# Kernel optimization log

Measured on AMD Instinct MI355X. Metric: run time of the kernel, lower is better.

## Reference

```python
import jax, jax.numpy as jnp
import numpy as np

ALPHA = 0.0  # module init alpha
BETA = 1.0   # default beta in set_target_with_data


def setup_inputs() -> dict:
    key = jax.random.key(0)
    k1, k2, k3, k4 = jax.random.split(key, 4)
    B, H, KP, N, D = 4, 16, 512, 4096, 64
    return {
        "K": jax.random.normal(k1, (B, H, KP, D), dtype=jnp.float32),
        "V": jax.random.normal(k2, (B, H, KP, D), dtype=jnp.float32),
        "xk": jax.random.normal(k3, (B, H, N, D), dtype=jnp.float32),
        "xv": jax.random.normal(k4, (B, H, N, D), dtype=jnp.float32),
    }


def reference(K, V, xk, xv):
    # set_target_with_data with dist_metric='dot', beta=1.0, beta2=None
    # dists: (B, H, k, n) = K @ xk^T
    dists = jnp.einsum('bhkd,bhnd->bhkn', K, xk)
    # softmax over the memory-slot axis (dim=-2)
    dk = jax.nn.softmax(BETA * dists, axis=-2)
    # normalize over the data axis (dim=-1)
    dkx = dk / jnp.sum(dk, axis=-1, keepdims=True)
    # weighted readout of data queries/values
    K_target = jnp.einsum('bhkn,bhnd->bhkd', dkx, xk)
    V_target = jnp.einsum('bhkn,bhnd->bhkd', dkx, xv)
    # set_target: grads used by maximize-SGD update
    gK = (1.0 - ALPHA) * (K_target - K)
    gV = (1.0 - ALPHA) * (V_target - V)
    return jnp.stack((gK, gV), axis=0)  # (2, B, H, k, d)
```

## Files before the change

### kernel.cpp

```cpp
#include <hip/hip_runtime.h>
#include <hip/hip_bf16.h>

typedef __bf16 bf16_t;
typedef __attribute__((ext_vector_type(8))) __bf16 bf16x8;
typedef __attribute__((ext_vector_type(4))) float f32x4;

#define BH 64
#define KP 512
#define NN 4096
#define DD 64
#define GSZ (BH * KP * DD)

#define MFMA16(a, b, c) __builtin_amdgcn_mfma_f32_16x16x32_bf16((a), (b), (c), 0, 0, 0)

__device__ __forceinline__ bf16x8 cvt8v(const f32x4 lo, const f32x4 hi) {
  bf16x8 r;
  r[0] = (bf16_t)lo[0]; r[1] = (bf16_t)lo[1]; r[2] = (bf16_t)lo[2]; r[3] = (bf16_t)lo[3];
  r[4] = (bf16_t)hi[0]; r[5] = (bf16_t)hi[1]; r[6] = (bf16_t)hi[2]; r[7] = (bf16_t)hi[3];
  return r;
}
__device__ __forceinline__ bf16x8 cvt8(const float* __restrict__ p) {
  return cvt8v(*(const f32x4*)p, *(const f32x4*)(p + 4));
}

__device__ __forceinline__ void stage16(bf16_t* lds_base, const bf16_t* gsrc) {
  __builtin_amdgcn_global_load_lds(
      (const __attribute__((address_space(1))) void*)gsrc,
      (__attribute__((address_space(3))) void*)lds_base, 16, 0, 0);
}

__global__ __launch_bounds__(256) void hop_prep(
    const float* __restrict__ xk, const float* __restrict__ xv,
    bf16_t* __restrict__ xk16, bf16_t* __restrict__ xkT16, bf16_t* __restrict__ xvT16)
{
  __shared__ __align__(16) bf16_t T[64 * 72];
  const int t = threadIdx.x;
  const int n0 = blockIdx.x * 64;
  const int bh = blockIdx.y;
  const int row = t >> 2;
  const int d0  = (t & 3) * 16;
  const int dcol = t >> 2;
  const int nb   = (t & 3) * 16;
  const size_t gb  = (size_t)bh * NN * DD;
  const size_t gbT = (size_t)bh * DD * NN;

  {
    const float* src = xk + gb + (size_t)(n0 + row) * DD + d0;
    const f32x4 a0 = *(const f32x4*)(src);
    const f32x4 a1 = *(const f32x4*)(src + 4);
    const f32x4 a2 = *(const f32x4*)(src + 8);
    const f32x4 a3 = *(const f32x4*)(src + 12);
    const bf16x8 lo = cvt8v(a0, a1), hi = cvt8v(a2, a3);
    bf16_t* dn = xk16 + gb + (size_t)(n0 + row) * DD + d0;
    *(bf16x8*)(dn)     = lo;
    *(bf16x8*)(dn + 8) = hi;
    *(bf16x8*)(T + row * 72 + d0)     = lo;
    *(bf16x8*)(T + row * 72 + d0 + 8) = hi;
  }
  __syncthreads();
  {
    bf16x8 o0, o1;
    #pragma unroll
    for (int j = 0; j < 8; j++) o0[j] = T[(nb + j) * 72 + dcol];
    #pragma unroll
    for (int j = 0; j < 8; j++) o1[j] = T[(nb + 8 + j) * 72 + dcol];
    bf16_t* dT = xkT16 + gbT + (size_t)dcol * NN + n0 + nb;
    *(bf16x8*)(dT)     = o0;
    *(bf16x8*)(dT + 8) = o1;
  }
  __syncthreads();
  {
    const float* src = xv + gb + (size_t)(n0 + row) * DD + d0;
    const f32x4 a0 = *(const f32x4*)(src);
    const f32x4 a1 = *(const f32x4*)(src + 4);
    const f32x4 a2 = *(const f32x4*)(src + 8);
    const f32x4 a3 = *(const f32x4*)(src + 12);
    *(bf16x8*)(T + row * 72 + d0)     = cvt8v(a0, a1);
    *(bf16x8*)(T + row * 72 + d0 + 8) = cvt8v(a2, a3);
  }
  __syncthreads();
  {
    bf16x8 o0, o1;
    #pragma unroll
    for (int j = 0; j < 8; j++) o0[j] = T[(nb + j) * 72 + dcol];
    #pragma unroll
    for (int j = 0; j < 8; j++) o1[j] = T[(nb + 8 + j) * 72 + dcol];
    bf16_t* dT = xvT16 + gbT + (size_t)dcol * NN + n0 + nb;
    *(bf16x8*)(dT)     = o0;
    *(bf16x8*)(dT + 8) = o1;
  }
}

__global__ __launch_bounds__(256) void hop_pass1(
    const float* __restrict__ Km, const bf16_t* __restrict__ xk16,
    float* __restrict__ inv_colsum)
{
  __shared__ __align__(16) bf16_t Ks[128 * 72];

  const int tid  = threadIdx.x;
  const int wave = tid >> 6, lane = tid & 63;
  const int col  = lane & 15, quad = lane >> 4;
  const int bid  = blockIdx.x;
  const int bh   = (bid & 7) + 8 * ((bid >> 3) & 7);
  const int n0   = (bid >> 6) * 256 + wave * 64;

  const float*  Kb   = Km   + (size_t)bh * KP * DD;
  const bf16_t* xkb  = xk16 + (size_t)bh * NN * DD;

  bf16x8 bf[4][2];
  #pragma unroll
  for (int nsub = 0; nsub < 4; nsub++) {
    const bf16_t* p = xkb + (size_t)(n0 + nsub * 16 + col) * DD + quad * 8;
    bf[nsub][0] = *(const bf16x8*)(p);
    bf[nsub][1] = *(const bf16x8*)(p + 32);
  }

  float colacc[4] = {0.f, 0.f, 0.f, 0.f};
  const int srow = tid >> 1, sdo = (tid & 1) * 32;

  for (int kc = 0; kc < KP; kc += 128) {
    __syncthreads();
    const float* src = Kb + (size_t)(kc + srow) * DD + sdo;
    #pragma unroll
    for (int u = 0; u < 4; u++) {
      const f32x4 p0 = *(const f32x4*)(src + 8 * u);
      const f32x4 p1 = *(const f32x4*)(src + 8 * u + 4);
      *(bf16x8*)(Ks + srow * 72 + sdo + 8 * u) = cvt8v(p0, p1);
    }
    __syncthreads();
    #pragma unroll
    for (int ks = 0; ks < 8; ks++) {
      const bf16x8 a0 = *(const bf16x8*)(Ks + (ks * 16 + col) * 72 + quad * 8);
      const bf16x8 a1 = *(const bf16x8*)(Ks + (ks * 16 + col) * 72 + 32 + quad * 8);
      #pragma unroll
      for (int nsub = 0; nsub < 4; nsub++) {
        f32x4 c = {0.f, 0.f, 0.f, 0.f};
        c = MFMA16(a0, bf[nsub][0], c);
        c = MFMA16(a1, bf[nsub][1], c);
        colacc[nsub] += __expf(c[0]) + __expf(c[1]) + __expf(c[2]) + __expf(c[3]);
      }
    }
  }
  #pragma unroll
  for (int nsub = 0; nsub < 4; nsub++) {
    colacc[nsub] += __shfl_xor(colacc[nsub], 16, 64);
    colacc[nsub] += __shfl_xor(colacc[nsub], 32, 64);
  }
  float v = colacc[0];
  v = (quad == 1) ? colacc[1] : v;
  v = (quad == 2) ? colacc[2] : v;
  v = (quad == 3) ? colacc[3] : v;
  inv_colsum[bh * NN + n0 + quad * 16 + col] = 1.0f / v;
}

#define NT 64
#define PW 72

__global__ __launch_bounds__(256) void hop_pass2(
    const float* __restrict__ Km, const float* __restrict__ Vm,
    const bf16_t* __restrict__ xk16, const bf16_t* __restrict__ xkT16,
    const bf16_t* __restrict__ xvT16,
    const float* __restrict__ inv_colsum, float* __restrict__ out)
{
  __shared__ __align__(16) bf16_t xks[2][NT * DD];
  __shared__ __align__(16) bf16_t xkT[2][DD * NT];
  __shared__ __align__(16) bf16_t xvT[2][DD * NT];
  __shared__ __align__(16) bf16_t wt[4][16 * PW];

  const int tid  = threadIdx.x;
  const int wave = tid >> 6, lane = tid & 63;
  const int col  = lane & 15, quad = lane >> 4;
  const int bid  = blockIdx.x;
  const int bh   = (bid & 7) + 8 * ((bid >> 3) & 7);
  const int k0   = (bid >> 6) * 64 + wave * 16;

  const float*  Kb   = Km    + (size_t)bh * KP * DD;
  const float*  Vb   = Vm    + (size_t)bh * KP * DD;
  const bf16_t* xkb  = xk16  + (size_t)bh * NN * DD;
  const bf16_t* xkTb = xkT16 + (size_t)bh * DD * NN;
  const bf16_t* xvTb = xvT16 + (size_t)bh * DD * NN;
  const float*  inv  = inv_colsum + bh * NN;

  const bf16x8 ak0 = cvt8(Kb + (size_t)(k0 + col) * DD + quad * 8);
  const bf16x8 ak1 = cvt8(Kb + (size_t)(k0 + col) * DD + 32 + quad * 8);

  f32x4 accK[4], accV[4];
  #pragma unroll
  for (int i = 0; i < 4; i++) {
    accK[i] = (f32x4){0.f, 0.f, 0.f, 0.f};
    accV[i] = (f32x4){0.f, 0.f, 0.f, 0.f};
  }
  float rows_part = 0.f;

  const int srl = lane >> 3;
  const int r0  = wave * 16 + srl;
  const int r1  = r0 + 8;
  const int sb  = ((lane & 7) ^ srl) * 8;
  const int lb0 = (wave * 2 + 0) * 512;
  const int lb1 = (wave * 2 + 1) * 512;

  stage16(&xks[0][lb0], xkb + (size_t)r0 * DD + sb);
  stage16(&xks[0][lb1], xkb + (size_t)r1 * DD + sb);
  stage16(&xkT[0][lb0], xkTb + (size_t)r0 * NN + sb);
  stage16(&xkT[0][lb1], xkTb + (size_t)r1 * NN + sb);
  stage16(&xvT[0][lb0], xvTb + (size_t)r0 * NN + sb);
  stage16(&xvT[0][lb1], xvTb + (size_t)r1 * NN + sb);
  __syncthreads();

  int cur = 0;
  for (int n0 = 0; n0 < NN; n0 += NT) {
    if (n0 + NT < NN) {
      const int nx = n0 + NT;
      const int nb = cur ^ 1;
      stage16(&xks[nb][lb0], xkb + (size_t)(nx + r0) * DD + sb);
      stage16(&xks[nb][lb1], xkb + (size_t)(nx + r1) * DD + sb);
      stage16(&xkT[nb][lb0], xkTb + (size_t)r0 * NN + nx + sb);
      stage16(&xkT[nb][lb1], xkTb + (size_t)r1 * NN + nx + sb);
      stage16(&xvT[nb][lb0], xvTb + (size_t)r0 * NN + nx + sb);
      stage16(&xvT[nb][lb1], xvTb + (size_t)r1 * NN + nx + sb);
    }

    float ic[4];
    #pragma unroll
    for (int ns = 0; ns < 4; ns++) ic[ns] = inv[n0 + ns * 16 + col];

    const int key = col & 7;

    f32x4 s[4];
    #pragma unroll
    for (int ns = 0; ns < 4; ns++) {
      const bf16_t* bp = &xks[cur][(ns * 16 + col) * DD];
      const bf16x8 b0 = *(const bf16x8*)(bp + 8 * (quad ^ key));
      const bf16x8 b1 = *(const bf16x8*)(bp + 8 * ((quad + 4) ^ key));
      f32x4 c = {0.f, 0.f, 0.f, 0.f};
      c = MFMA16(ak0, b0, c);
      c = MFMA16(ak1, b1, c);
      s[ns] = c;
    }
    bf16_t* wr = wt[wave];
    #pragma unroll
    for (int ns = 0; ns < 4; ns++) {
      #pragma unroll
      for (int r = 0; r < 4; r++)
        wr[(quad * 4 + r) * PW + ns * 16 + col] = (bf16_t)(__expf(s[ns][r]) * ic[ns]);
    }
    const bf16x8 wa0 = *(const bf16x8*)(wr + col * PW + quad * 8);
    const bf16x8 wa1 = *(const bf16x8*)(wr + col * PW + 32 + quad * 8);
    #pragma unroll
    for (int j = 0; j < 8; j++) rows_part += (float)wa0[j] + (float)wa1[j];

    #pragma unroll
    for (int dt = 0; dt < 4; dt++) {
      const int d = dt * 16 + col;
      const bf16_t* kp = &xkT[cur][d * NT];
      const bf16_t* vp = &xvT[cur][d * NT];
      const bf16x8 bk0 = *(const bf16x8*)(kp + 8 * (quad ^ key));
      const bf16x8 bk1 = *(const bf16x8*)(kp + 8 * ((quad + 4) ^ key));
      const bf16x8 bv0 = *(const bf16x8*)(vp + 8 * (quad ^ key));
      const bf16x8 bv1 = *(const bf16x8*)(vp + 8 * ((quad + 4) ^ key));
      accK[dt] = MFMA16(wa0, bk0, accK[dt]);
      accK[dt] = MFMA16(wa1, bk1, accK[dt]);
      accV[dt] = MFMA16(wa0, bv0, accV[dt]);
      accV[dt] = MFMA16(wa1, bv1, accV[dt]);
    }

    __syncthreads();
    cur ^= 1;
  }

  float rs = rows_part;
  rs += __shfl_xor(rs, 16, 64);
  rs += __shfl_xor(rs, 32, 64);
  float invrs[4];
  #pragma unroll
  for (int r = 0; r < 4; r++) invrs[r] = 1.0f / __shfl(rs, quad * 4 + r, 64);

  const size_t base = (size_t)bh * KP * DD;
  #pragma unroll
  for (int dt = 0; dt < 4; dt++) {
    #pragma unroll
    for (int r = 0; r < 4; r++) {
      const int k = k0 + quad * 4 + r;
      const int d = dt * 16 + col;
      const size_t idx = base + (size_t)k * DD + d;
      out[idx]       = accK[dt][r] * invrs[r] - Kb[(size_t)k * DD + d];
      out[GSZ + idx] = accV[dt][r] * invrs[r] - Vb[(size_t)k * DD + d];
    }
  }
}

__global__ __launch_bounds__(256) void hop_pass1_fb(
    const float* __restrict__ Km, const float* __restrict__ xk,
    float* __restrict__ inv_colsum)
{
  __shared__ __align__(16) bf16_t Ks[128 * 72];
  const int tid  = threadIdx.x;
  const int wave = tid >> 6, lane = tid & 63;
  const int col  = lane & 15, quad = lane >> 4;
  const int bh = blockIdx.y;
  const int n0 = blockIdx.x * 256 + wave * 64;
  const float* Kb  = Km + (size_t)bh * KP * DD;
  const float* xkb = xk + (size_t)bh * NN * DD;
  bf16x8 bf[4][2];
  #pragma unroll
  for (int nsub = 0; nsub < 4; nsub++) {
    const float* p = xkb + (size_t)(n0 + nsub * 16 + col) * DD + quad * 8;
    bf[nsub][0] = cvt8(p);
    bf[nsub][1] = cvt8(p + 32);
  }
  float colacc[4] = {0.f, 0.f, 0.f, 0.f};
  const int srow = tid >> 1, sdo = (tid & 1) * 32;
  for (int kc = 0; kc < KP; kc += 128) {
    __syncthreads();
    const float* src = Kb + (size_t)(kc + srow) * DD + sdo;
    #pragma unroll
    for (int u = 0; u < 4; u++) {
      const f32x4 p0 = *(const f32x4*)(src + 8 * u);
      const f32x4 p1 = *(const f32x4*)(src + 8 * u + 4);
      *(bf16x8*)(Ks + srow * 72 + sdo + 8 * u) = cvt8v(p0, p1);
    }
    __syncthreads();
    #pragma unroll
    for (int ks = 0; ks < 8; ks++) {
      const bf16x8 a0 = *(const bf16x8*)(Ks + (ks * 16 + col) * 72 + quad * 8);
      const bf16x8 a1 = *(const bf16x8*)(Ks + (ks * 16 + col) * 72 + 32 + quad * 8);
      #pragma unroll
      for (int nsub = 0; nsub < 4; nsub++) {
        f32x4 c = {0.f, 0.f, 0.f, 0.f};
        c = MFMA16(a0, bf[nsub][0], c);
        c = MFMA16(a1, bf[nsub][1], c);
        colacc[nsub] += __expf(c[0]) + __expf(c[1]) + __expf(c[2]) + __expf(c[3]);
      }
    }
  }
  #pragma unroll
  for (int nsub = 0; nsub < 4; nsub++) {
    colacc[nsub] += __shfl_xor(colacc[nsub], 16, 64);
    colacc[nsub] += __shfl_xor(colacc[nsub], 32, 64);
  }
  float v = colacc[0];
  v = (quad == 1) ? colacc[1] : v;
  v = (quad == 2) ? colacc[2] : v;
  v = (quad == 3) ? colacc[3] : v;
  inv_colsum[bh * NN + n0 + quad * 16 + col] = 1.0f / v;
}

__global__ __launch_bounds__(256) void hop_pass2_fb(
    const float* __restrict__ Km, const float* __restrict__ Vm,
    const float* __restrict__ xk, const float* __restrict__ xv,
    const float* __restrict__ inv_colsum, float* __restrict__ out)
{
  __shared__ __align__(16) bf16_t xksf[NT * PW];
  __shared__ __align__(16) bf16_t xkTf[DD * NT];
  __shared__ __align__(16) bf16_t xvTf[DD * NT];
  __shared__ __align__(16) bf16_t wtf[4][16 * PW];

  const int tid  = threadIdx.x;
  const int wave = tid >> 6, lane = tid & 63;
  const int col  = lane & 15, quad = lane >> 4;
  const int bh   = blockIdx.x >> 3;
  const int k0   = (blockIdx.x & 7) * 64 + wave * 16;

  const float* Kb  = Km + (size_t)bh * KP * DD;
  const float* Vb  = Vm + (size_t)bh * KP * DD;
  const float* xkb = xk + (size_t)bh * NN * DD;
  const float* xvb = xv + (size_t)bh * NN * DD;
  const float* inv = inv_colsum + bh * NN;

  const bf16x8 ak0 = cvt8(Kb + (size_t)(k0 + col) * DD + quad * 8);
  const bf16x8 ak1 = cvt8(Kb + (size_t)(k0 + col) * DD + 32 + quad * 8);

  f32x4 accK[4], accV[4];
  #pragma unroll
  for (int i = 0; i < 4; i++) {
    accK[i] = (f32x4){0.f, 0.f, 0.f, 0.f};
    accV[i] = (f32x4){0.f, 0.f, 0.f, 0.f};
  }
  float rows_part = 0.f;

  const int sn = tid >> 2;
  const int sd = (tid & 3) * 16;
  const int shi = sn >> 3, slo = sn & 7;

  for (int n0 = 0; n0 < NN; n0 += NT) {
    f32x4 gk[4], gv[4];
    #pragma unroll
    for (int u = 0; u < 4; u++) {
      gk[u] = *(const f32x4*)(xkb + (size_t)(n0 + sn) * DD + sd + 4 * u);
      gv[u] = *(const f32x4*)(xvb + (size_t)(n0 + sn) * DD + sd + 4 * u);
    }
    float ic[4];
    #pragma unroll
    for (int nsub = 0; nsub < 4; nsub++) ic[nsub] = inv[n0 + nsub * 16 + col];

    __syncthreads();
    *(bf16x8*)(xksf + sn * PW + sd)     = cvt8v(gk[0], gk[1]);
    *(bf16x8*)(xksf + sn * PW + sd + 8) = cvt8v(gk[2], gk[3]);
    #pragma unroll
    for (int j = 0; j < 16; j++) {
      const int d   = sd + j;
      const int off = d * NT + (((shi) ^ (d >> 3)) << 3) + slo;
      xkTf[off] = (bf16_t)gk[j >> 2][j & 3];
      xvTf[off] = (bf16_t)gv[j >> 2][j & 3];
    }
    __syncthreads();

    f32x4 s[4];
    #pragma unroll
    for (int nsub = 0; nsub < 4; nsub++) {
      const bf16x8 b0 = *(const bf16x8*)(xksf + (nsub * 16 + col) * PW + quad * 8);
      const bf16x8 b1 = *(const bf16x8*)(xksf + (nsub * 16 + col) * PW + 32 + quad * 8);
      f32x4 c = {0.f, 0.f, 0.f, 0.f};
      c = MFMA16(ak0, b0, c);
      c = MFMA16(ak1, b1, c);
      s[nsub] = c;
    }
    bf16_t* wr = wtf[wave];
    #pragma unroll
    for (int nsub = 0; nsub < 4; nsub++) {
      #pragma unroll
      for (int r = 0; r < 4; r++)
        wr[(quad * 4 + r) * PW + nsub * 16 + col] = (bf16_t)(__expf(s[nsub][r]) * ic[nsub]);
    }
    const bf16x8 wa0 = *(const bf16x8*)(wr + col * PW + quad * 8);
    const bf16x8 wa1 = *(const bf16x8*)(wr + col * PW + 32 + quad * 8);
    #pragma unroll
    for (int j = 0; j < 8; j++) rows_part += (float)wa0[j] + (float)wa1[j];

    #pragma unroll
    for (int dt = 0; dt < 4; dt++) {
      const int d = dt * 16 + col, dhi = d >> 3;
      const bf16x8 bk0 = *(const bf16x8*)(xkTf + d * NT + ((quad ^ dhi) << 3));
      const bf16x8 bk1 = *(const bf16x8*)(xkTf + d * NT + (((4 + quad) ^ dhi) << 3));
      const bf16x8 bv0 = *(const bf16x8*)(xvTf + d * NT + ((quad ^ dhi) << 3));
      const bf16x8 bv1 = *(const bf16x8*)(xvTf + d * NT + (((4 + quad) ^ dhi) << 3));
      accK[dt] = MFMA16(wa0, bk0, accK[dt]);
      accK[dt] = MFMA16(wa1, bk1, accK[dt]);
      accV[dt] = MFMA16(wa0, bv0, accV[dt]);
      accV[dt] = MFMA16(wa1, bv1, accV[dt]);
    }
  }

  float rs = rows_part;
  rs += __shfl_xor(rs, 16, 64);
  rs += __shfl_xor(rs, 32, 64);
  float invrs[4];
  #pragma unroll
  for (int r = 0; r < 4; r++) invrs[r] = 1.0f / __shfl(rs, quad * 4 + r, 64);

  const size_t base = (size_t)bh * KP * DD;
  #pragma unroll
  for (int dt = 0; dt < 4; dt++) {
    #pragma unroll
    for (int r = 0; r < 4; r++) {
      const int k = k0 + quad * 4 + r;
      const int d = dt * 16 + col;
      const size_t idx = base + (size_t)k * DD + d;
      out[idx]       = accK[dt][r] * invrs[r] - Kb[(size_t)k * DD + d];
      out[GSZ + idx] = accV[dt][r] * invrs[r] - Vb[(size_t)k * DD + d];
    }
  }
}

extern "C" void kernel_launch(void* const* d_in, const int* in_sizes, int n_in,
                              void* d_out, int out_size, void* d_ws, size_t ws_size,
                              hipStream_t stream)
{
  (void)in_sizes; (void)n_in; (void)out_size;
  const float* Km = (const float*)d_in[0];
  const float* Vm = (const float*)d_in[1];
  const float* xk = (const float*)d_in[2];
  const float* xv = (const float*)d_in[3];
  float* out = (float*)d_out;
  float* inv_colsum = (float*)d_ws;

  const size_t SCRE = (size_t)BH * NN * DD;
  const size_t NEED = (size_t)BH * NN * sizeof(float) + 3 * SCRE * sizeof(bf16_t);

  if (ws_size >= NEED) {
    bf16_t* xk16  = (bf16_t*)((char*)d_ws + (size_t)BH * NN * sizeof(float));
    bf16_t* xkT16 = xk16 + SCRE;
    bf16_t* xvT16 = xkT16 + SCRE;
    hop_prep<<<dim3(NN / 64, BH), 256, 0, stream>>>(xk, xv, xk16, xkT16, xvT16);
    hop_pass1<<<dim3((NN / 256) * BH), 256, 0, stream>>>(Km, xk16, inv_colsum);
    hop_pass2<<<dim3(BH * (KP / 64)), 256, 0, stream>>>(Km, Vm, xk16, xkT16, xvT16,
                                                        inv_colsum, out);
  } else {
    hop_pass1_fb<<<dim3(NN / 256, BH), 256, 0, stream>>>(Km, xk, inv_colsum);
    hop_pass2_fb<<<dim3(BH * (KP / 64)), 256, 0, stream>>>(Km, Vm, xk, xv,
                                                           inv_colsum, out);
  }
}
```

Before: 306.4 us.

## Fuse bf16 prep/transpose into pass1 with whole-K LDS staging

Merges the xk/xv bf16 conversion and transpose kernel into the column-sum pass. Each block handles 512 data rows of one head, converts and transposes them, then stages all of K in LDS once and computes the exp column sums. This drops one kernel launch and stops K from being reloaded per 256-column block. In exchange it uses a much larger LDS footprint (about 72KB), which lowers occupancy. The prep work also runs serially before the MFMA work inside each block, and the grid shrinks to 512 blocks.

```diff
diff --git a/kernel.cpp b/kernel.cpp
--- a/kernel.cpp
+++ b/kernel.cpp
@@ -29,128 +29,133 @@
       (__attribute__((address_space(3))) void*)lds_base, 16, 0, 0);
 }
 
-__global__ __launch_bounds__(256) void hop_prep(
-    const float* __restrict__ xk, const float* __restrict__ xv,
-    bf16_t* __restrict__ xk16, bf16_t* __restrict__ xkT16, bf16_t* __restrict__ xvT16)
+__global__ __launch_bounds__(256) void hop_pass1f(
+    const float* __restrict__ Km, const float* __restrict__ xk,
+    const float* __restrict__ xv,
+    bf16_t* __restrict__ xk16, bf16_t* __restrict__ xkT16,
+    bf16_t* __restrict__ xvT16, float* __restrict__ inv_colsum)
 {
-  __shared__ __align__(16) bf16_t T[64 * 72];
-  const int t = threadIdx.x;
-  const int n0 = blockIdx.x * 64;
-  const int bh = blockIdx.y;
-  const int row = t >> 2;
-  const int d0  = (t & 3) * 16;
-  const int dcol = t >> 2;
-  const int nb   = (t & 3) * 16;
-  const size_t gb  = (size_t)bh * NN * DD;
-  const size_t gbT = (size_t)bh * DD * NN;
-
-  {
-    const float* src = xk + gb + (size_t)(n0 + row) * DD + d0;
-    const f32x4 a0 = *(const f32x4*)(src);
-    const f32x4 a1 = *(const f32x4*)(src + 4);
-    const f32x4 a2 = *(const f32x4*)(src + 8);
-    const f32x4 a3 = *(const f32x4*)(src + 12);
-    const bf16x8 lo = cvt8v(a0, a1), hi = cvt8v(a2, a3);
-    bf16_t* dn = xk16 + gb + (size_t)(n0 + row) * DD + d0;
-    *(bf16x8*)(dn)     = lo;
-    *(bf16x8*)(dn + 8) = hi;
-    *(bf16x8*)(T + row * 72 + d0)     = lo;
-    *(bf16x8*)(T + row * 72 + d0 + 8) = hi;
-  }
-  __syncthreads();
-  {
-    bf16x8 o0, o1;
-    #pragma unroll
-    for (int j = 0; j < 8; j++) o0[j] = T[(nb + j) * 72 + dcol];
-    #pragma unroll
-    for (int j = 0; j < 8; j++) o1[j] = T[(nb + 8 + j) * 72 + dcol];
-    bf16_t* dT = xkT16 + gbT + (size_t)dcol * NN + n0 + nb;
-    *(bf16x8*)(dT)     = o0;
-    *(bf16x8*)(dT + 8) = o1;
-  }
-  __syncthreads();
-  {
-    const float* src = xv + gb + (size_t)(n0 + row) * DD + d0;
-    const f32x4 a0 = *(const f32x4*)(src);
-    const f32x4 a1 = *(const f32x4*)(src + 4);
-    const f32x4 a2 = *(const f32x4*)(src + 8);
-    const f32x4 a3 = *(const f32x4*)(src + 12);
-    *(bf16x8*)(T + row * 72 + d0)     = cvt8v(a0, a1);
-    *(bf16x8*)(T + row * 72 + d0 + 8) = cvt8v(a2, a3);
-  }
-  __syncthreads();
-  {
-    bf16x8 o0, o1;
-    #pragma unroll
-    for (int j = 0; j < 8; j++) o0[j] = T[(nb + j) * 72 + dcol];
-    #pragma unroll
-    for (int j = 0; j < 8; j++) o1[j] = T[(nb + 8 + j) * 72 + dcol];
-    bf16_t* dT = xvT16 + gbT + (size_t)dcol * NN + n0 + nb;
-    *(bf16x8*)(dT)     = o0;
-    *(bf16x8*)(dT + 8) = o1;
-  }
-}
-
-__global__ __launch_bounds__(256) void hop_pass1(
-    const float* __restrict__ Km, const bf16_t* __restrict__ xk16,
-    float* __restrict__ inv_colsum)
-{
-  __shared__ __align__(16) bf16_t Ks[128 * 72];
+  __shared__ __align__(16) bf16_t Ks[512 * 72];
 
   const int tid  = threadIdx.x;
   const int wave = tid >> 6, lane = tid & 63;
   const int col  = lane & 15, quad = lane >> 4;
   const int bid  = blockIdx.x;
   const int bh   = (bid & 7) + 8 * ((bid >> 3) & 7);
-  const int n0   = (bid >> 6) * 256 + wave * 64;
-
-  const float*  Kb   = Km   + (size_t)bh * KP * DD;
-  const bf16_t* xkb  = xk16 + (size_t)bh * NN * DD;
-
-  bf16x8 bf[4][2];
-  #pragma unroll
-  for (int nsub = 0; nsub < 4; nsub++) {
-    const bf16_t* p = xkb + (size_t)(n0 + nsub * 16 + col) * DD + quad * 8;
-    bf[nsub][0] = *(const bf16x8*)(p);
-    bf[nsub][1] = *(const bf16x8*)(p + 32);
-  }
-
-  float colacc[4] = {0.f, 0.f, 0.f, 0.f};
-  const int srow = tid >> 1, sdo = (tid & 1) * 32;
-
-  for (int kc = 0; kc < KP; kc += 128) {
-    __syncthreads();
-    const float* src = Kb + (size_t)(kc + srow) * DD + sdo;
-    #pragma unroll
-    for (int u = 0; u < 4; u++) {
-      const f32x4 p0 = *(const f32x4*)(src + 8 * u);
-      const f32x4 p1 = *(const f32x4*)(src + 8 * u + 4);
-      *(bf16x8*)(Ks + srow * 72 + sdo + 8 * u) = cvt8v(p0, p1);
-    }
-    __syncthreads();
-    #pragma unroll
-    for (int ks = 0; ks < 8; ks++) {
+  const int nblk = (bid >> 6) * 512;
+
+  const float* Kb  = Km + (size_t)bh * KP * DD;
+  const float* xkb = xk + (size_t)bh * NN * DD + (size_t)nblk * DD;
+  const float* xvb = xv + (size_t)bh * NN * DD + (size_t)nblk * DD;
+  bf16_t* xk16b = xk16  + (size_t)bh * NN * DD + (size_t)nblk * DD;
+  bf16_t* xkTb  = xkT16 + (size_t)bh * DD * NN + nblk;
+  bf16_t* xvTb  = xvT16 + (size_t)bh * DD * NN + nblk;
+
+  bf16_t* T = Ks;
+
+  const int row  = tid >> 2;
+  const int d0   = (tid & 3) * 16;
+  const int dcol = tid >> 2;
+  const int nb   = (tid & 3) * 16;
+
+  for (int b = 0; b < 8; b++) {
+    {
+      const float* src = xkb + (size_t)(b * 64 + row) * DD + d0;
+      const f32x4 a0 = *(const f32x4*)(src);
+      const f32x4 a1 = *(const f32x4*)(src + 4);
+      const f32x4 a2 = *(const f32x4*)(src + 8);
+      const f32x4 a3 = *(const f32x4*)(src + 12);
+      const bf16x8 lo = cvt8v(a0, a1), hi = cvt8v(a2, a3);
+      bf16_t* dn = xk16b + (size_t)(b * 64 + row) * DD + d0;
+      *(bf16x8*)(dn)     = lo;
+      *(bf16x8*)(dn + 8) = hi;
+      *(bf16x8*)(T + row * 72 + d0)     = lo;
+      *(bf16x8*)(T + row * 72 + d0 + 8) = hi;
+    }
+    __syncthreads();
+    {
+      bf16x8 o0, o1;
+      #pragma unroll
+      for (int j = 0; j < 8; j++) o0[j] = T[(nb + j) * 72 + dcol];
+      #pragma unroll
+      for (int j = 0; j < 8; j++) o1[j] = T[(nb + 8 + j) * 72 + dcol];
+      bf16_t* dT = xkTb + (size_t)dcol * NN + b * 64 + nb;
+      *(bf16x8*)(dT)     = o0;
+      *(bf16x8*)(dT + 8) = o1;
+    }
+    __syncthreads();
+    {
+      const float* src = xvb + (size_t)(b * 64 + row) * DD + d0;
+      const f32x4 a0 = *(const f32x4*)(src);
+      const f32x4 a1 = *(const f32x4*)(src + 4);
+      const f32x4 a2 = *(const f32x4*)(src + 8);
+      const f32x4 a3 = *(const f32x4*)(src + 12);
+      *(bf16x8*)(T + row * 72 + d0)     = cvt8v(a0, a1);
+      *(bf16x8*)(T + row * 72 + d0 + 8) = cvt8v(a2, a3);
+    }
+    __syncthreads();
+    {
+      bf16x8 o0, o1;
+      #pragma unroll
+      for (int j = 0; j < 8; j++) o0[j] = T[(nb + j) * 72 + dcol];
+      #pragma unroll
+      for (int j = 0; j < 8; j++) o1[j] = T[(nb + 8 + j) * 72 + dcol];
+      bf16_t* dT = xvTb + (size_t)dcol * NN + b * 64 + nb;
+      *(bf16x8*)(dT)     = o0;
+      *(bf16x8*)(dT + 8) = o1;
+    }
+    __syncthreads();
+  }
+
+  {
+    const int srow = tid >> 1, sdo = (tid & 1) * 32;
+    #pragma unroll
+    for (int kc = 0; kc < KP; kc += 128) {
+      const float* src = Kb + (size_t)(kc + srow) * DD + sdo;
+      #pragma unroll
+      for (int u = 0; u < 4; u++) {
+        const f32x4 p0 = *(const f32x4*)(src + 8 * u);
+        const f32x4 p1 = *(const f32x4*)(src + 8 * u + 4);
+        *(bf16x8*)(Ks + (size_t)(kc + srow) * 72 + sdo + 8 * u) = cvt8v(p0, p1);
+      }
+    }
+  }
+  __syncthreads();
+
+  #pragma unroll
+  for (int t = 0; t < 2; t++) {
+    const int n0 = wave * 128 + t * 64;
+    bf16x8 bfr[4][2];
+    #pragma unroll
+    for (int nsub = 0; nsub < 4; nsub++) {
+      const bf16_t* p = xk16b + (size_t)(n0 + nsub * 16 + col) * DD + quad * 8;
+      bfr[nsub][0] = *(const bf16x8*)(p);
+      bfr[nsub][1] = *(const bf16x8*)(p + 32);
+    }
+    float colacc[4] = {0.f, 0.f, 0.f, 0.f};
+    #pragma unroll 4
+    for (int ks = 0; ks < 32; ks++) {
       const bf16x8 a0 = *(const bf16x8*)(Ks + (ks * 16 + col) * 72 + quad * 8);
       const bf16x8 a1 = *(const bf16x8*)(Ks + (ks * 16 + col) * 72 + 32 + quad * 8);
       #pragma unroll
       for (int nsub = 0; nsub < 4; nsub++) {
         f32x4 c = {0.f, 0.f, 0.f, 0.f};
-        c = MFMA16(a0, bf[nsub][0], c);
-        c = MFMA16(a1, bf[nsub][1], c);
+        c = MFMA16(a0, bfr[nsub][0], c);
+        c = MFMA16(a1, bfr[nsub][1], c);
         colacc[nsub] += __expf(c[0]) + __expf(c[1]) + __expf(c[2]) + __expf(c[3]);
       }
     }
-  }
-  #pragma unroll
-  for (int nsub = 0; nsub < 4; nsub++) {
-    colacc[nsub] += __shfl_xor(colacc[nsub], 16, 64);
-    colacc[nsub] += __shfl_xor(colacc[nsub], 32, 64);
-  }
-  float v = colacc[0];
-  v = (quad == 1) ? colacc[1] : v;
-  v = (quad == 2) ? colacc[2] : v;
-  v = (quad == 3) ? colacc[3] : v;
-  inv_colsum[bh * NN + n0 + quad * 16 + col] = 1.0f / v;
+    #pragma unroll
+    for (int nsub = 0; nsub < 4; nsub++) {
+      colacc[nsub] += __shfl_xor(colacc[nsub], 16, 64);
+      colacc[nsub] += __shfl_xor(colacc[nsub], 32, 64);
+    }
+    float v = colacc[0];
+    v = (quad == 1) ? colacc[1] : v;
+    v = (quad == 2) ? colacc[2] : v;
+    v = (quad == 3) ? colacc[3] : v;
+    inv_colsum[bh * NN + nblk + n0 + quad * 16 + col] = 1.0f / v;
+  }
 }
 
 #define NT 64
@@ -211,13 +216,13 @@
   for (int n0 = 0; n0 < NN; n0 += NT) {
     if (n0 + NT < NN) {
       const int nx = n0 + NT;
-      const int nb = cur ^ 1;
-      stage16(&xks[nb][lb0], xkb + (size_t)(nx + r0) * DD + sb);
-      stage16(&xks[nb][lb1], xkb + (size_t)(nx + r1) * DD + sb);
-      stage16(&xkT[nb][lb0], xkTb + (size_t)r0 * NN + nx + sb);
-      stage16(&xkT[nb][lb1], xkTb + (size_t)r1 * NN + nx + sb);
-      stage16(&xvT[nb][lb0], xvTb + (size_t)r0 * NN + nx + sb);
-      stage16(&xvT[nb][lb1], xvTb + (size_t)r1 * NN + nx + sb);
+      const int nb2 = cur ^ 1;
+      stage16(&xks[nb2][lb0], xkb + (size_t)(nx + r0) * DD + sb);
+      stage16(&xks[nb2][lb1], xkb + (size_t)(nx + r1) * DD + sb);
+      stage16(&xkT[nb2][lb0], xkTb + (size_t)r0 * NN + nx + sb);
+      stage16(&xkT[nb2][lb1], xkTb + (size_t)r1 * NN + nx + sb);
+      stage16(&xvT[nb2][lb0], xvTb + (size_t)r0 * NN + nx + sb);
+      stage16(&xvT[nb2][lb1], xvTb + (size_t)r1 * NN + nx + sb);
     }
 
     float ic[4];
@@ -481,8 +486,8 @@
     bf16_t* xk16  = (bf16_t*)((char*)d_ws + (size_t)BH * NN * sizeof(float));
     bf16_t* xkT16 = xk16 + SCRE;
     bf16_t* xvT16 = xkT16 + SCRE;
-    hop_prep<<<dim3(NN / 64, BH), 256, 0, stream>>>(xk, xv, xk16, xkT16, xvT16);
-    hop_pass1<<<dim3((NN / 256) * BH), 256, 0, stream>>>(Km, xk16, inv_colsum);
+    hop_pass1f<<<dim3(512), 256, 0, stream>>>(Km, xk, xv, xk16, xkT16, xvT16,
+                                              inv_colsum);
     hop_pass2<<<dim3(BH * (KP / 64)), 256, 0, stream>>>(Km, Vm, xk16, xkT16, xvT16,
                                                         inv_colsum, out);
   } else {
```

Result: no change. 311.3 us (+1.6%).

## Use 32x32 MFMA in pass2 with register permlane weight transpose

Applied to the files above, without the earlier changes.

Rewrites the second pass to use 32x32x16 bf16 MFMA with each wave covering 32 memory rows. Scores are computed transposed so the exp weights can be rearranged into the A-operand layout with v_permlane32_swap instead of round-tripping through LDS. Each block handles 128 rows, which halves how often data tiles are reloaded per row, but also halves the grid size and raises register use.

```diff
diff --git a/kernel.cpp b/kernel.cpp
--- a/kernel.cpp
+++ b/kernel.cpp
@@ -4,6 +4,7 @@
 typedef __bf16 bf16_t;
 typedef __attribute__((ext_vector_type(8))) __bf16 bf16x8;
 typedef __attribute__((ext_vector_type(4))) float f32x4;
+typedef __attribute__((ext_vector_type(16))) float f32x16;
 
 #define BH 64
 #define KP 512
@@ -12,6 +13,7 @@
 #define GSZ (BH * KP * DD)
 
 #define MFMA16(a, b, c) __builtin_amdgcn_mfma_f32_16x16x32_bf16((a), (b), (c), 0, 0, 0)
+#define MFMA32(a, b, c) __builtin_amdgcn_mfma_f32_32x32x16_bf16((a), (b), (c), 0, 0, 0)
 
 __device__ __forceinline__ bf16x8 cvt8v(const f32x4 lo, const f32x4 hi) {
   bf16x8 r;
@@ -21,6 +23,11 @@
 }
 __device__ __forceinline__ bf16x8 cvt8(const float* __restrict__ p) {
   return cvt8v(*(const f32x4*)p, *(const f32x4*)(p + 4));
+}
+__device__ __forceinline__ unsigned pack2(float a, float b) {
+  union { bf16_t h[2]; unsigned u; } x;
+  x.h[0] = (bf16_t)a; x.h[1] = (bf16_t)b;
+  return x.u;
 }
 
 __device__ __forceinline__ void stage16(bf16_t* lds_base, const bf16_t* gsrc) {
@@ -154,7 +161,6 @@
 }
 
 #define NT 64
-#define PW 72
 
 __global__ __launch_bounds__(256) void hop_pass2(
     const float* __restrict__ Km, const float* __restrict__ Vm,
@@ -165,14 +171,16 @@
   __shared__ __align__(16) bf16_t xks[2][NT * DD];
   __shared__ __align__(16) bf16_t xkT[2][DD * NT];
   __shared__ __align__(16) bf16_t xvT[2][DD * NT];
-  __shared__ __align__(16) bf16_t wt[4][16 * PW];
+  __shared__ float rows_lds[4][32];
 
   const int tid  = threadIdx.x;
   const int wave = tid >> 6, lane = tid & 63;
-  const int col  = lane & 15, quad = lane >> 4;
+  const int col  = lane & 31, hi = lane >> 5;
   const int bid  = blockIdx.x;
-  const int bh   = (bid & 7) + 8 * ((bid >> 3) & 7);
-  const int k0   = (bid >> 6) * 64 + wave * 16;
+  const int m    = bid >> 3;
+  const int bh   = (bid & 7) + 8 * (m >> 2);
+  const int kblk = m & 3;
+  const int k0w  = kblk * 128 + wave * 32;
 
   const float*  Kb   = Km    + (size_t)bh * KP * DD;
   const float*  Vb   = Vm    + (size_t)bh * KP * DD;
@@ -181,16 +189,18 @@
   const bf16_t* xvTb = xvT16 + (size_t)bh * DD * NN;
   const float*  inv  = inv_colsum + bh * NN;
 
-  const bf16x8 ak0 = cvt8(Kb + (size_t)(k0 + col) * DD + quad * 8);
-  const bf16x8 ak1 = cvt8(Kb + (size_t)(k0 + col) * DD + 32 + quad * 8);
-
-  f32x4 accK[4], accV[4];
-  #pragma unroll
-  for (int i = 0; i < 4; i++) {
-    accK[i] = (f32x4){0.f, 0.f, 0.f, 0.f};
-    accV[i] = (f32x4){0.f, 0.f, 0.f, 0.f};
-  }
-  float rows_part = 0.f;
+  bf16x8 bk[4];
+  #pragma unroll
+  for (int t = 0; t < 4; t++)
+    bk[t] = cvt8(Kb + (size_t)(k0w + col) * DD + t * 16 + hi * 8);
+
+  f32x16 accK[2], accV[2];
+  #pragma unroll
+  for (int i = 0; i < 2; i++) {
+    #pragma unroll
+    for (int r = 0; r < 16; r++) { accK[i][r] = 0.f; accV[i][r] = 0.f; }
+  }
+  float rowacc = 0.f;
 
   const int srl = lane >> 3;
   const int r0  = wave * 16 + srl;
@@ -211,83 +221,92 @@
   for (int n0 = 0; n0 < NN; n0 += NT) {
     if (n0 + NT < NN) {
       const int nx = n0 + NT;
-      const int nb = cur ^ 1;
-      stage16(&xks[nb][lb0], xkb + (size_t)(nx + r0) * DD + sb);
-      stage16(&xks[nb][lb1], xkb + (size_t)(nx + r1) * DD + sb);
-      stage16(&xkT[nb][lb0], xkTb + (size_t)r0 * NN + nx + sb);
-      stage16(&xkT[nb][lb1], xkTb + (size_t)r1 * NN + nx + sb);
-      stage16(&xvT[nb][lb0], xvTb + (size_t)r0 * NN + nx + sb);
-      stage16(&xvT[nb][lb1], xvTb + (size_t)r1 * NN + nx + sb);
-    }
-
-    float ic[4];
-    #pragma unroll
-    for (int ns = 0; ns < 4; ns++) ic[ns] = inv[n0 + ns * 16 + col];
-
-    const int key = col & 7;
-
-    f32x4 s[4];
-    #pragma unroll
-    for (int ns = 0; ns < 4; ns++) {
-      const bf16_t* bp = &xks[cur][(ns * 16 + col) * DD];
-      const bf16x8 b0 = *(const bf16x8*)(bp + 8 * (quad ^ key));
-      const bf16x8 b1 = *(const bf16x8*)(bp + 8 * ((quad + 4) ^ key));
-      f32x4 c = {0.f, 0.f, 0.f, 0.f};
-      c = MFMA16(ak0, b0, c);
-      c = MFMA16(ak1, b1, c);
-      s[ns] = c;
-    }
-    bf16_t* wr = wt[wave];
-    #pragma unroll
-    for (int ns = 0; ns < 4; ns++) {
-      #pragma unroll
-      for (int r = 0; r < 4; r++)
-        wr[(quad * 4 + r) * PW + ns * 16 + col] = (bf16_t)(__expf(s[ns][r]) * ic[ns]);
-    }
-    const bf16x8 wa0 = *(const bf16x8*)(wr + col * PW + quad * 8);
-    const bf16x8 wa1 = *(const bf16x8*)(wr + col * PW + 32 + quad * 8);
-    #pragma unroll
-    for (int j = 0; j < 8; j++) rows_part += (float)wa0[j] + (float)wa1[j];
-
-    #pragma unroll
-    for (int dt = 0; dt < 4; dt++) {
-      const int d = dt * 16 + col;
-      const bf16_t* kp = &xkT[cur][d * NT];
-      const bf16_t* vp = &xvT[cur][d * NT];
-      const bf16x8 bk0 = *(const bf16x8*)(kp + 8 * (quad ^ key));
-      const bf16x8 bk1 = *(const bf16x8*)(kp + 8 * ((quad + 4) ^ key));
-      const bf16x8 bv0 = *(const bf16x8*)(vp + 8 * (quad ^ key));
-      const bf16x8 bv1 = *(const bf16x8*)(vp + 8 * ((quad + 4) ^ key));
-      accK[dt] = MFMA16(wa0, bk0, accK[dt]);
-      accK[dt] = MFMA16(wa1, bk1, accK[dt]);
-      accV[dt] = MFMA16(wa0, bv0, accV[dt]);
-      accV[dt] = MFMA16(wa1, bv1, accV[dt]);
+      const int nb2 = cur ^ 1;
+      stage16(&xks[nb2][lb0], xkb + (size_t)(nx + r0) * DD + sb);
+      stage16(&xks[nb2][lb1], xkb + (size_t)(nx + r1) * DD + sb);
+      stage16(&xkT[nb2][lb0], xkTb + (size_t)r0 * NN + nx + sb);
+      stage16(&xkT[nb2][lb1], xkTb + (size_t)r1 * NN + nx + sb);
+      stage16(&xvT[nb2][lb0], xvTb + (size_t)r0 * NN + nx + sb);
+      stage16(&xvT[nb2][lb1], xvTb + (size_t)r1 * NN + nx + sb);
+    }
+
+    const bf16_t* xs = xks[cur];
+    bf16x8 wa[4];
+
+    #pragma unroll
+    for (int nh = 0; nh < 2; nh++) {
+      f32x4 icv[4];
+      #pragma unroll
+      for (int q = 0; q < 4; q++)
+        icv[q] = *(const f32x4*)(inv + n0 + 32 * nh + 8 * q + 4 * hi);
+
+      const int n  = nh * 32 + col;
+      const int rb = n * DD;
+      f32x16 s;
+      #pragma unroll
+      for (int r = 0; r < 16; r++) s[r] = 0.f;
+      #pragma unroll
+      for (int t = 0; t < 4; t++) {
+        const bf16x8 a = *(const bf16x8*)(xs + rb + (((2 * t + hi) ^ (n & 7)) << 3));
+        s = MFMA32(a, bk[t], s);
+      }
+      #pragma unroll
+      for (int b = 0; b < 2; b++) {
+        float p[8];
+        #pragma unroll
+        for (int j = 0; j < 8; j++)
+          p[j] = __expf(s[8 * b + j]) * icv[2 * b + (j >> 2)][j & 3];
+        rowacc += ((p[0] + p[1]) + (p[2] + p[3])) + ((p[4] + p[5]) + (p[6] + p[7]));
+        unsigned q0a = pack2(p[0], p[1]), q0b = pack2(p[2], p[3]);
+        unsigned q1a = pack2(p[4], p[5]), q1b = pack2(p[6], p[7]);
+        asm("v_permlane32_swap_b32 %0, %1" : "+v"(q0a), "+v"(q1a));
+        asm("v_permlane32_swap_b32 %0, %1" : "+v"(q0b), "+v"(q1b));
+        union { unsigned u[4]; bf16x8 v; } f;
+        f.u[0] = q0a; f.u[1] = q0b; f.u[2] = q1a; f.u[3] = q1b;
+        wa[nh * 2 + b] = f.v;
+      }
+    }
+
+    #pragma unroll
+    for (int dg = 0; dg < 2; dg++) {
+      const int d   = dg * 32 + col;
+      const int rbd = d * NT;
+      const bf16_t* kp = xkT[cur];
+      const bf16_t* vp = xvT[cur];
+      #pragma unroll
+      for (int c = 0; c < 4; c++) {
+        const int off = rbd + (((2 * c + hi) ^ (d & 7)) << 3);
+        const bf16x8 bkf = *(const bf16x8*)(kp + off);
+        const bf16x8 bvf = *(const bf16x8*)(vp + off);
+        accK[dg] = MFMA32(wa[c], bkf, accK[dg]);
+        accV[dg] = MFMA32(wa[c], bvf, accV[dg]);
+      }
     }
 
     __syncthreads();
     cur ^= 1;
   }
 
-  float rs = rows_part;
-  rs += __shfl_xor(rs, 16, 64);
-  rs += __shfl_xor(rs, 32, 64);
-  float invrs[4];
-  #pragma unroll
-  for (int r = 0; r < 4; r++) invrs[r] = 1.0f / __shfl(rs, quad * 4 + r, 64);
+  rowacc += __shfl_xor(rowacc, 32, 64);
+  rows_lds[wave][col] = 1.0f / rowacc;
 
   const size_t base = (size_t)bh * KP * DD;
   #pragma unroll
-  for (int dt = 0; dt < 4; dt++) {
-    #pragma unroll
-    for (int r = 0; r < 4; r++) {
-      const int k = k0 + quad * 4 + r;
-      const int d = dt * 16 + col;
+  for (int dg = 0; dg < 2; dg++) {
+    #pragma unroll
+    for (int r = 0; r < 16; r++) {
+      const int kw = (r & 3) + 8 * (r >> 2) + 4 * hi;
+      const float invr = rows_lds[wave][kw];
+      const int k = k0w + kw;
+      const int d = dg * 32 + col;
       const size_t idx = base + (size_t)k * DD + d;
-      out[idx]       = accK[dt][r] * invrs[r] - Kb[(size_t)k * DD + d];
-      out[GSZ + idx] = accV[dt][r] * invrs[r] - Vb[(size_t)k * DD + d];
-    }
-  }
-}
+      out[idx]       = accK[dg][r] * invr - Kb[(size_t)k * DD + d];
+      out[GSZ + idx] = accV[dg][r] * invr - Vb[(size_t)k * DD + d];
+    }
+  }
+}
+
+#define PW 72
 
 __global__ __launch_bounds__(256) void hop_pass1_fb(
     const float* __restrict__ Km, const float* __restrict__ xk,
@@ -483,8 +502,8 @@
     bf16_t* xvT16 = xkT16 + SCRE;
     hop_prep<<<dim3(NN / 64, BH), 256, 0, stream>>>(xk, xv, xk16, xkT16, xvT16);
     hop_pass1<<<dim3((NN / 256) * BH), 256, 0, stream>>>(Km, xk16, inv_colsum);
-    hop_pass2<<<dim3(BH * (KP / 64)), 256, 0, stream>>>(Km, Vm, xk16, xkT16, xvT16,
-                                                        inv_colsum, out);
+    hop_pass2<<<dim3(BH * 4), 256, 0, stream>>>(Km, Vm, xk16, xkT16, xvT16,
+                                                inv_colsum, out);
   } else {
     hop_pass1_fb<<<dim3(NN / 256, BH), 256, 0, stream>>>(Km, xk, inv_colsum);
     hop_pass2_fb<<<dim3(BH * (KP / 64)), 256, 0, stream>>>(Km, Vm, xk, xv,
```

Result: slower. 329.7 us (+7.6%).
